# Kernel optimization log

Hardware: AMD Instinct MI355X
Metric: run time of the kernel (lower is better)

## Reference

```python
import jax, jax.numpy as jnp
import numpy as np

D, N, L = 1024, 128, 128
B, S = 4, 4096

def setup_inputs() -> dict:
    key = jax.random.key(0)
    kx, kq, kk, kv = jax.random.split(key, 4)
    x = jax.random.normal(kx, (B, S, D), dtype=jnp.float32)
    # nn.Linear(d, n, bias=False) weight has shape [n, d]; y = x @ W.T
    Wq = jax.random.normal(kq, (N, D), dtype=jnp.float32) * (1.0 / np.sqrt(D))
    Wk = jax.random.normal(kk, (N, D), dtype=jnp.float32) * (1.0 / np.sqrt(D))
    Wv = jax.random.normal(kv, (L, D), dtype=jnp.float32) * (1.0 / np.sqrt(D))
    return {"x": x, "Wq": Wq, "Wk": Wk, "Wv": Wv}

def reference(x, Wq, Wk, Wv):
    scale = jnp.sqrt(jnp.asarray(D, dtype=x.dtype))  # self.d = sqrt(d) in source
    q = jnp.einsum('bsd,nd->bsn', x, Wq)  # [B,S,N]
    k = jnp.einsum('bsd,nd->bsn', x, Wk)  # [B,S,N]
    v = jnp.einsum('bsd,ld->bsl', x, Wv)  # [B,S,L]
    scores = jnp.einsum('bqn,bkn->bqk', q, k) / scale  # [B,S,S]
    a = jax.nn.softmax(scores, axis=-1)
    return jnp.einsum('bqk,bkl->bql', a, v)  # [B,S,L]
```

## Files before the change

kernel.cpp:

```cpp
#include <hip/hip_runtime.h>
#include <stdint.h>

typedef __attribute__((ext_vector_type(8))) _Float16 f16x8;
typedef __attribute__((ext_vector_type(4))) float f32x4;
typedef __attribute__((ext_vector_type(2))) float f32x2;

#define S_ 4096
#define D_ 1024
#define NROWS 16384

__global__ __launch_bounds__(256) void gemm_qkv(
    const float* __restrict__ x, const float* __restrict__ Wq,
    const float* __restrict__ Wk, const float* __restrict__ Wv,
    _Float16* __restrict__ qk, _Float16* __restrict__ vt)
{
  __shared__ char smem[32768];
  float* At = (float*)smem;
  float* Bt = (float*)(smem + 16384);
  const int tid  = threadIdx.x;
  const int lane = tid & 63, wid = tid >> 6;
  const int g = lane >> 4, l15 = lane & 15;
  const int wr = wid >> 1, wc = wid & 1;
  const int m0 = blockIdx.x * 128;
  const int by = blockIdx.y;
  const float* W = (by == 0) ? Wq : ((by == 1) ? Wk : Wv);

  f32x4 acc[4][4] = {};

  for (int k0 = 0; k0 < D_; k0 += 32) {
    #pragma unroll
    for (int it = 0; it < 4; ++it) {
      int G   = it * 256 + tid;
      int row = G >> 3;
      int cb  = ((G & 7) ^ (row & 7)) << 4;
      const char* ga = (const char*)x + (size_t)(m0 + row) * 4096 + k0 * 4 + cb;
      const char* gb = (const char*)W + (size_t)row * 4096 + k0 * 4 + cb;
      __builtin_amdgcn_global_load_lds(ga, (char*)At + (it * 256 + wid * 64) * 16, 16, 0, 0);
      __builtin_amdgcn_global_load_lds(gb, (char*)Bt + (it * 256 + wid * 64) * 16, 16, 0, 0);
    }
    __syncthreads();

    f16x8 af[4], bg[4];
    #pragma unroll
    for (int mt = 0; mt < 4; ++mt) {
      int row = wr * 64 + mt * 16 + l15;
      const char* base = (const char*)At + row * 128;
      f32x4 a0 = *(const f32x4*)(base + (((2 * g    ) ^ (row & 7)) << 4));
      f32x4 a1 = *(const f32x4*)(base + (((2 * g + 1) ^ (row & 7)) << 4));
      #pragma unroll
      for (int i = 0; i < 4; ++i) { af[mt][i] = (_Float16)a0[i]; af[mt][i + 4] = (_Float16)a1[i]; }
    }
    #pragma unroll
    for (int nt = 0; nt < 4; ++nt) {
      int row = wc * 64 + nt * 16 + l15;
      const char* base = (const char*)Bt + row * 128;
      f32x4 b0 = *(const f32x4*)(base + (((2 * g    ) ^ (row & 7)) << 4));
      f32x4 b1 = *(const f32x4*)(base + (((2 * g + 1) ^ (row & 7)) << 4));
      #pragma unroll
      for (int i = 0; i < 4; ++i) { bg[nt][i] = (_Float16)b0[i]; bg[nt][i + 4] = (_Float16)b1[i]; }
    }

    __builtin_amdgcn_s_setprio(1);
    #pragma unroll
    for (int mt = 0; mt < 4; ++mt)
      #pragma unroll
      for (int nt = 0; nt < 4; ++nt)
        acc[mt][nt] = __builtin_amdgcn_mfma_f32_16x16x32_f16(af[mt], bg[nt], acc[mt][nt], 0, 0, 0);
    __builtin_amdgcn_s_setprio(0);
    __syncthreads();
  }

  if (by < 2) {
    #pragma unroll
    for (int mt = 0; mt < 4; ++mt)
      #pragma unroll
      for (int nt = 0; nt < 4; ++nt)
        #pragma unroll
        for (int r = 0; r < 4; ++r) {
          int row = m0 + wr * 64 + mt * 16 + (g << 2) + r;
          int col = by * 128 + wc * 64 + nt * 16 + l15;
          qk[(size_t)row * 256 + col] = (_Float16)acc[mt][nt][r];
        }
  } else {
    _Float16* T = (_Float16*)smem;
    #pragma unroll
    for (int mt = 0; mt < 4; ++mt)
      #pragma unroll
      for (int nt = 0; nt < 4; ++nt)
        #pragma unroll
        for (int r = 0; r < 4; ++r)
          T[(wr * 64 + mt * 16 + (g << 2) + r) * 128 + wc * 64 + nt * 16 + l15] =
              (_Float16)acc[mt][nt][r];
    __syncthreads();
    const int b = m0 >> 12, s_base = m0 & 4095;
    #pragma unroll
    for (int it = 0; it < 8; ++it) {
      int Wn = it * 256 + tid;
      int f = Wn >> 4, S64 = (Wn >> 3) & 1, gran = Wn & 7;
      int kk = gran >> 2, q = gran & 3;
      f16x8 v;
      #pragma unroll
      for (int i = 0; i < 8; ++i) {
        int h = i >> 2, j = i & 3;
        int sl = S64 * 64 + kk * 32 + h * 16 + q * 4 + j;
        v[i] = T[sl * 128 + f];
      }
      *(f16x8*)((char*)vt + (size_t)(b * 128 + f) * 8192 + s_base * 2 + S64 * 128 + gran * 16) = v;
    }
  }
}

__global__ __launch_bounds__(512, 4) void attn(const _Float16* __restrict__ qk,
                                               const _Float16* __restrict__ vt,
                                               _Float16* __restrict__ pO,
                                               float* __restrict__ pml,
                                               int ntiles)
{
  __shared__ _Float16 K0l[64 * 128], K1l[64 * 128];
  __shared__ _Float16 V0l[64 * 128], V1l[64 * 128];
  const int tid  = threadIdx.x;
  const int lane = tid & 63, wid = tid >> 6;
  const int g = lane >> 4, l15 = lane & 15;
  const int b  = blockIdx.y;
  const int q0 = blockIdx.x * 128;
  const int split = blockIdx.z;
  const int kv_begin = split * (ntiles * 64);

  f16x8 qf[4];
  {
    const size_t qrow = (size_t)(b * S_ + q0 + wid * 16 + l15) * 256;
    #pragma unroll
    for (int kk = 0; kk < 4; ++kk)
      qf[kk] = *(const f16x8*)(qk + qrow + kk * 32 + g * 8);
  }

  const char* gK[2]; const char* gV[2];
  #pragma unroll
  for (int it = 0; it < 2; ++it) {
    int G = it * 512 + tid;
    int row = G >> 4, ch = G & 15;
    gK[it] = (const char*)qk + (size_t)(b * S_ + kv_begin + row) * 512 + 256 +
             (((ch << 4)) ^ ((row & 15) << 4));
    int f = G >> 3, c = G & 7;
    gV[it] = (const char*)vt + (size_t)(b * 128 + f) * 8192 + (kv_begin >> 6) * 128 +
             ((c ^ (f & 7)) << 4);
  }

#define STAGE(Kb, Vb) do {                                                          \
    _Pragma("unroll")                                                               \
    for (int it_ = 0; it_ < 2; ++it_) {                                             \
      __builtin_amdgcn_global_load_lds(gK[it_],                                     \
          (char*)(Kb) + (it_ * 512 + wid * 64) * 16, 16, 0, 0);                     \
      __builtin_amdgcn_global_load_lds(gV[it_],                                     \
          (char*)(Vb) + (it_ * 512 + wid * 64) * 16, 16, 0, 0);                     \
    }                                                                               \
    gK[0] += 32768; gK[1] += 32768; gV[0] += 128; gV[1] += 128;                     \
  } while (0)

  f32x4 oacc[8] = {};
  float m_run = -1e30f, l_run = 0.f;

#define COMPUTE(Kb, Vb) do {                                                        \
    f32x4 sacc[4] = {};                                                             \
    __builtin_amdgcn_s_setprio(1);                                                  \
    _Pragma("unroll")                                                               \
    for (int kk = 0; kk < 4; ++kk) {                                                \
      const char* kb = (const char*)(Kb) + l15 * 256 +                              \
                       (((kk << 6) | (g << 4)) ^ (l15 << 4));                       \
      _Pragma("unroll")                                                             \
      for (int kvt = 0; kvt < 4; ++kvt) {                                           \
        f16x8 kf = *(const f16x8*)(kb + kvt * 4096);                                \
        sacc[kvt] = __builtin_amdgcn_mfma_f32_16x16x32_f16(kf, qf[kk], sacc[kvt],   \
                                                           0, 0, 0);                \
      }                                                                             \
    }                                                                               \
    __builtin_amdgcn_s_setprio(0);                                                  \
    float pmax = -1e30f;                                                            \
    _Pragma("unroll")                                                               \
    for (int kvt = 0; kvt < 4; ++kvt)                                               \
      _Pragma("unroll")                                                             \
      for (int r = 0; r < 4; ++r) {                                                 \
        float s = sacc[kvt][r] * 0.03125f;                                          \
        sacc[kvt][r] = s;                                                           \
        pmax = fmaxf(pmax, s);                                                      \
      }                                                                             \
    pmax = fmaxf(pmax, __shfl_xor(pmax, 16));                                       \
    pmax = fmaxf(pmax, __shfl_xor(pmax, 32));                                       \
    if (!__all(pmax - m_run <= 5.5f)) {                                             \
      float m_new = fmaxf(m_run, pmax);                                             \
      float corr  = __expf(m_run - m_new);                                          \
      l_run *= corr;                                                                \
      m_run  = m_new;                                                               \
      _Pragma("unroll")                                                             \
      for (int r = 0; r < 4; ++r) {                                                 \
        float cr = __builtin_bit_cast(float,                                        \
            __builtin_amdgcn_ds_bpermute((((g << 2) + r) << 2),                     \
                                         __builtin_bit_cast(int, corr)));           \
        _Pragma("unroll")                                                           \
        for (int ft = 0; ft < 8; ++ft) oacc[ft][r] *= cr;                           \
      }                                                                             \
    }                                                                               \
    float psum = 0.f;                                                               \
    f16x8 pa[2];                                                                    \
    _Pragma("unroll")                                                               \
    for (int k2 = 0; k2 < 2; ++k2)                                                  \
      _Pragma("unroll")                                                             \
      for (int i = 0; i < 8; ++i) {                                                 \
        float p = __expf(sacc[2 * k2 + (i >> 2)][i & 3] - m_run);                   \
        psum += p;                                                                  \
        pa[k2][i] = (_Float16)p;                                                    \
      }                                                                             \
    psum += __shfl_xor(psum, 16);                                                   \
    psum += __shfl_xor(psum, 32);                                                   \
    l_run += psum;                                                                  \
    __builtin_amdgcn_s_setprio(1);                                                  \
    _Pragma("unroll")                                                               \
    for (int k2 = 0; k2 < 2; ++k2) {                                                \
      const char* vb = (const char*)(Vb) + l15 * 128 +                              \
                       (((k2 << 6) | (g << 4)) ^ ((l15 & 7) << 4));                 \
      _Pragma("unroll")                                                             \
      for (int ft = 0; ft < 8; ++ft) {                                              \
        f16x8 vf = *(const f16x8*)(vb + ft * 2048);                                 \
        oacc[ft] = __builtin_amdgcn_mfma_f32_16x16x32_f16(pa[k2], vf, oacc[ft],     \
                                                          0, 0, 0);                 \
      }                                                                             \
    }                                                                               \
    __builtin_amdgcn_s_setprio(0);                                                  \
  } while (0)

  STAGE(K0l, V0l);
  __syncthreads();
  for (int t = 0; t < ntiles; t += 2) {
    STAGE(K1l, V1l);
    COMPUTE(K0l, V0l);
    __syncthreads();
    if (t + 2 < ntiles) STAGE(K0l, V0l);
    COMPUTE(K1l, V1l);
    __syncthreads();
  }

  #pragma unroll
  for (int r = 0; r < 4; ++r) {
    float mr = __builtin_bit_cast(float,
                 __builtin_amdgcn_ds_bpermute((((g << 2) + r) << 2),
                                              __builtin_bit_cast(int, m_run)));
    float lr = __builtin_bit_cast(float,
                 __builtin_amdgcn_ds_bpermute((((g << 2) + r) << 2),
                                              __builtin_bit_cast(int, l_run)));
    float inv = 1.f / lr;
    const int grow = b * S_ + q0 + wid * 16 + (g << 2) + r;
    _Float16* od = pO + ((size_t)split * NROWS + grow) * 128;
    #pragma unroll
    for (int ft = 0; ft < 8; ++ft)
      od[ft * 16 + l15] = (_Float16)(oacc[ft][r] * inv);
    if (l15 == 0)
      *(f32x2*)(pml + ((size_t)split * NROWS + grow) * 2) = f32x2{mr, lr};
  }
#undef STAGE
#undef COMPUTE
}

__global__ __launch_bounds__(256) void combine(const _Float16* __restrict__ pO,
                                               const float* __restrict__ pml,
                                               float* __restrict__ out,
                                               int nsplit)
{
  const int tid = threadIdx.x;
  const int row = blockIdx.x * 2 + (tid >> 7);
  const int col = tid & 127;

  float M = -1e30f;
  for (int s = 0; s < nsplit; ++s)
    M = fmaxf(M, pml[((size_t)s * NROWS + row) * 2]);
  float den = 0.f, num = 0.f;
  for (int s = 0; s < nsplit; ++s) {
    f32x2 ml = *(const f32x2*)(pml + ((size_t)s * NROWS + row) * 2);
    float w = __expf(ml.x - M) * ml.y;
    den += w;
    num += w * (float)pO[((size_t)s * NROWS + row) * 128 + col];
  }
  out[(size_t)row * 128 + col] = num / den;
}

extern "C" void kernel_launch(void* const* d_in, const int* in_sizes, int n_in,
                              void* d_out, int out_size, void* d_ws, size_t ws_size,
                              hipStream_t stream)
{
  (void)in_sizes; (void)n_in; (void)out_size;
  const float* x  = (const float*)d_in[0];
  const float* Wq = (const float*)d_in[1];
  const float* Wk = (const float*)d_in[2];
  const float* Wv = (const float*)d_in[3];

  char* ws = (char*)d_ws;
  _Float16* qkbuf = (_Float16*)ws;
  _Float16* vtbuf = (_Float16*)(ws + (size_t)NROWS * 256 * 2);
  const size_t base  = (size_t)NROWS * 256 * 2 + (size_t)4 * 128 * 4096 * 2;
  const size_t perO  = (size_t)NROWS * 128 * 2;
  const size_t perML = (size_t)NROWS * 2 * 4;

  int nsplit = 4;
  while (nsplit > 1 && base + (size_t)nsplit * (perO + perML) > ws_size) nsplit >>= 1;

  _Float16* pO  = (_Float16*)(ws + base);
  float*    pml = (float*)(ws + base + (size_t)nsplit * perO);
  float*    out = (float*)d_out;

  dim3 gg(128, 3);
  gemm_qkv<<<gg, 256, 0, stream>>>(x, Wq, Wk, Wv, qkbuf, vtbuf);
  dim3 ga(S_ / 128, 4, nsplit);
  attn<<<ga, 512, 0, stream>>>(qkbuf, vtbuf, pO, pml, 64 / nsplit);
  combine<<<NROWS / 2, 256, 0, stream>>>(pO, pml, out, nsplit);
}
```

Baseline: 102.1 us.

## Double-buffer QKV projection GEMM and halve its M tile to 64 rows

Restructures the QKV projection GEMM to use two LDS buffers, so the async global-to-LDS loads for the next K slice are issued before the MFMA compute on the current one. This removes the load-then-compute serialization of the old loop. The M tile shrinks from 128 to 64 rows, giving 768 blocks instead of 384 to fill the GPU better, with each wave now computing a 64x32 sub-tile. In exchange, the block uses more LDS (48KB), has less reuse of each loaded W tile, and reads W twice as often overall.

```diff
diff --git a/kernel.cpp b/kernel.cpp
--- a/kernel.cpp
+++ b/kernel.cpp
@@ -14,71 +14,99 @@
     const float* __restrict__ Wk, const float* __restrict__ Wv,
     _Float16* __restrict__ qk, _Float16* __restrict__ vt)
 {
-  __shared__ char smem[32768];
-  float* At = (float*)smem;
-  float* Bt = (float*)(smem + 16384);
+  __shared__ char smem[49152];
+  char* Ab[2] = { smem,        smem + 24576 };
+  char* Bb[2] = { smem + 8192, smem + 32768 };
   const int tid  = threadIdx.x;
   const int lane = tid & 63, wid = tid >> 6;
   const int g = lane >> 4, l15 = lane & 15;
-  const int wr = wid >> 1, wc = wid & 1;
-  const int m0 = blockIdx.x * 128;
+  const int m0 = blockIdx.x * 64;
   const int by = blockIdx.y;
   const float* W = (by == 0) ? Wq : ((by == 1) ? Wk : Wv);
 
-  f32x4 acc[4][4] = {};
-
-  for (int k0 = 0; k0 < D_; k0 += 32) {
-    #pragma unroll
-    for (int it = 0; it < 4; ++it) {
-      int G   = it * 256 + tid;
-      int row = G >> 3;
-      int cb  = ((G & 7) ^ (row & 7)) << 4;
-      const char* ga = (const char*)x + (size_t)(m0 + row) * 4096 + k0 * 4 + cb;
-      const char* gb = (const char*)W + (size_t)row * 4096 + k0 * 4 + cb;
-      __builtin_amdgcn_global_load_lds(ga, (char*)At + (it * 256 + wid * 64) * 16, 16, 0, 0);
-      __builtin_amdgcn_global_load_lds(gb, (char*)Bt + (it * 256 + wid * 64) * 16, 16, 0, 0);
-    }
-    __syncthreads();
-
-    f16x8 af[4], bg[4];
-    #pragma unroll
-    for (int mt = 0; mt < 4; ++mt) {
-      int row = wr * 64 + mt * 16 + l15;
-      const char* base = (const char*)At + row * 128;
-      f32x4 a0 = *(const f32x4*)(base + (((2 * g    ) ^ (row & 7)) << 4));
-      f32x4 a1 = *(const f32x4*)(base + (((2 * g + 1) ^ (row & 7)) << 4));
-      #pragma unroll
-      for (int i = 0; i < 4; ++i) { af[mt][i] = (_Float16)a0[i]; af[mt][i + 4] = (_Float16)a1[i]; }
-    }
-    #pragma unroll
-    for (int nt = 0; nt < 4; ++nt) {
-      int row = wc * 64 + nt * 16 + l15;
-      const char* base = (const char*)Bt + row * 128;
-      f32x4 b0 = *(const f32x4*)(base + (((2 * g    ) ^ (row & 7)) << 4));
-      f32x4 b1 = *(const f32x4*)(base + (((2 * g + 1) ^ (row & 7)) << 4));
-      #pragma unroll
-      for (int i = 0; i < 4; ++i) { bg[nt][i] = (_Float16)b0[i]; bg[nt][i + 4] = (_Float16)b1[i]; }
-    }
-
-    __builtin_amdgcn_s_setprio(1);
+  const char* pA[2]; const char* pB[4];
+  #pragma unroll
+  for (int it = 0; it < 2; ++it) {
+    int G = it * 256 + tid, row = G >> 3, gg = (G & 7) ^ (row & 7);
+    pA[it] = (const char*)x + (size_t)(m0 + row) * 4096 + gg * 16;
+  }
+  #pragma unroll
+  for (int it = 0; it < 4; ++it) {
+    int G = it * 256 + tid, row = G >> 3, gg = (G & 7) ^ (row & 7);
+    pB[it] = (const char*)W + (size_t)row * 4096 + gg * 16;
+  }
+
+#define GSTAGE(bi) do {                                                        \
+    _Pragma("unroll")                                                          \
+    for (int it_ = 0; it_ < 2; ++it_) {                                        \
+      __builtin_amdgcn_global_load_lds(pA[it_],                                \
+          Ab[bi] + (it_ * 256 + wid * 64) * 16, 16, 0, 0);                     \
+      pA[it_] += 128;                                                          \
+    }                                                                          \
+    _Pragma("unroll")                                                          \
+    for (int it_ = 0; it_ < 4; ++it_) {                                        \
+      __builtin_amdgcn_global_load_lds(pB[it_],                                \
+          Bb[bi] + (it_ * 256 + wid * 64) * 16, 16, 0, 0);                     \
+      pB[it_] += 128;                                                          \
+    }                                                                          \
+  } while (0)
+
+  f32x4 acc[4][2] = {};
+
+#define GCOMPUTE(bi) do {                                                      \
+    f16x8 af[4], bg[2];                                                        \
+    _Pragma("unroll")                                                          \
+    for (int mt = 0; mt < 4; ++mt) {                                           \
+      int row = mt * 16 + l15;                                                 \
+      const char* base = Ab[bi] + row * 128;                                   \
+      f32x4 a0 = *(const f32x4*)(base + (((2 * g    ) ^ (row & 7)) << 4));     \
+      f32x4 a1 = *(const f32x4*)(base + (((2 * g + 1) ^ (row & 7)) << 4));     \
+      _Pragma("unroll")                                                        \
+      for (int i = 0; i < 4; ++i) {                                            \
+        af[mt][i] = (_Float16)a0[i]; af[mt][i + 4] = (_Float16)a1[i];          \
+      }                                                                        \
+    }                                                                          \
+    _Pragma("unroll")                                                          \
+    for (int nt = 0; nt < 2; ++nt) {                                           \
+      int row = wid * 32 + nt * 16 + l15;                                      \
+      const char* base = Bb[bi] + row * 128;                                   \
+      f32x4 b0 = *(const f32x4*)(base + (((2 * g    ) ^ (row & 7)) << 4));     \
+      f32x4 b1 = *(const f32x4*)(base + (((2 * g + 1) ^ (row & 7)) << 4));     \
+      _Pragma("unroll")                                                        \
+      for (int i = 0; i < 4; ++i) {                                            \
+        bg[nt][i] = (_Float16)b0[i]; bg[nt][i + 4] = (_Float16)b1[i];          \
+      }                                                                        \
+    }                                                                          \
+    __builtin_amdgcn_s_setprio(1);                                             \
+    _Pragma("unroll")                                                          \
+    for (int mt = 0; mt < 4; ++mt)                                             \
+      _Pragma("unroll")                                                        \
+      for (int nt = 0; nt < 2; ++nt)                                           \
+        acc[mt][nt] = __builtin_amdgcn_mfma_f32_16x16x32_f16(af[mt], bg[nt],   \
+                                                             acc[mt][nt], 0, 0, 0); \
+    __builtin_amdgcn_s_setprio(0);                                             \
+  } while (0)
+
+  GSTAGE(0);
+  __syncthreads();
+  for (int t = 0; t < 32; t += 2) {
+    GSTAGE(1);
+    GCOMPUTE(0);
+    __syncthreads();
+    if (t + 2 < 32) GSTAGE(0);
+    GCOMPUTE(1);
+    __syncthreads();
+  }
+
+  if (by < 2) {
     #pragma unroll
     for (int mt = 0; mt < 4; ++mt)
       #pragma unroll
-      for (int nt = 0; nt < 4; ++nt)
-        acc[mt][nt] = __builtin_amdgcn_mfma_f32_16x16x32_f16(af[mt], bg[nt], acc[mt][nt], 0, 0, 0);
-    __builtin_amdgcn_s_setprio(0);
-    __syncthreads();
-  }
-
-  if (by < 2) {
-    #pragma unroll
-    for (int mt = 0; mt < 4; ++mt)
-      #pragma unroll
-      for (int nt = 0; nt < 4; ++nt)
+      for (int nt = 0; nt < 2; ++nt)
         #pragma unroll
         for (int r = 0; r < 4; ++r) {
-          int row = m0 + wr * 64 + mt * 16 + (g << 2) + r;
-          int col = by * 128 + wc * 64 + nt * 16 + l15;
+          int row = m0 + mt * 16 + (g << 2) + r;
+          int col = by * 128 + wid * 32 + nt * 16 + l15;
           qk[(size_t)row * 256 + col] = (_Float16)acc[mt][nt][r];
         }
   } else {
@@ -86,28 +114,29 @@
     #pragma unroll
     for (int mt = 0; mt < 4; ++mt)
       #pragma unroll
-      for (int nt = 0; nt < 4; ++nt)
+      for (int nt = 0; nt < 2; ++nt)
         #pragma unroll
         for (int r = 0; r < 4; ++r)
-          T[(wr * 64 + mt * 16 + (g << 2) + r) * 128 + wc * 64 + nt * 16 + l15] =
+          T[(mt * 16 + (g << 2) + r) * 128 + wid * 32 + nt * 16 + l15] =
               (_Float16)acc[mt][nt][r];
     __syncthreads();
     const int b = m0 >> 12, s_base = m0 & 4095;
     #pragma unroll
-    for (int it = 0; it < 8; ++it) {
+    for (int it = 0; it < 4; ++it) {
       int Wn = it * 256 + tid;
-      int f = Wn >> 4, S64 = (Wn >> 3) & 1, gran = Wn & 7;
+      int f = Wn >> 3, gran = Wn & 7;
       int kk = gran >> 2, q = gran & 3;
       f16x8 v;
       #pragma unroll
       for (int i = 0; i < 8; ++i) {
         int h = i >> 2, j = i & 3;
-        int sl = S64 * 64 + kk * 32 + h * 16 + q * 4 + j;
-        v[i] = T[sl * 128 + f];
+        v[i] = T[(kk * 32 + h * 16 + q * 4 + j) * 128 + f];
       }
-      *(f16x8*)((char*)vt + (size_t)(b * 128 + f) * 8192 + s_base * 2 + S64 * 128 + gran * 16) = v;
+      *(f16x8*)((char*)vt + (size_t)(b * 128 + f) * 8192 + s_base * 2 + gran * 16) = v;
     }
   }
+#undef GSTAGE
+#undef GCOMPUTE
 }
 
 __global__ __launch_bounds__(512, 4) void attn(const _Float16* __restrict__ qk,
@@ -306,7 +335,7 @@
   float*    pml = (float*)(ws + base + (size_t)nsplit * perO);
   float*    out = (float*)d_out;
 
-  dim3 gg(128, 3);
+  dim3 gg(256, 3);
   gemm_qkv<<<gg, 256, 0, stream>>>(x, Wq, Wk, Wv, qkbuf, vtbuf);
   dim3 ga(S_ / 128, 4, nsplit);
   attn<<<ga, 512, 0, stream>>>(qkbuf, vtbuf, pO, pml, 64 / nsplit);
```

New measurement: 92.44 us. -9.5%, faster.
